# Optimization experiments

Hardware: AMD Instinct MI355X
Metric: run time of the kernel (lower is better)

Reference implementation:

```python
import jax, jax.numpy as jnp
import numpy as np


def _bilinear_align_corners(g, H, W):
    # g: [B, 1, h, w] -> [B, 1, H, W], matching F.interpolate(mode='bilinear', align_corners=True)
    B, C, h, w = g.shape
    ys = jnp.linspace(0.0, h - 1.0, H)
    xs = jnp.linspace(0.0, w - 1.0, W)
    y0 = jnp.clip(jnp.floor(ys).astype(jnp.int32), 0, h - 1)
    y1 = jnp.clip(y0 + 1, 0, h - 1)
    x0 = jnp.clip(jnp.floor(xs).astype(jnp.int32), 0, w - 1)
    x1 = jnp.clip(x0 + 1, 0, w - 1)
    wy = (ys - y0.astype(g.dtype))[:, None]          # [H,1]
    wx = (xs - x0.astype(g.dtype))[None, :]          # [1,W]
    g00 = g[:, :, y0][:, :, :, x0]                   # [B,C,H,W]
    g01 = g[:, :, y0][:, :, :, x1]
    g10 = g[:, :, y1][:, :, :, x0]
    g11 = g[:, :, y1][:, :, :, x1]
    top = g00 * (1 - wx) + g01 * wx
    bot = g10 * (1 - wx) + g11 * wx
    return top * (1 - wy) + bot * wy


def setup_inputs() -> dict:
    key = jax.random.key(0)
    ks = jax.random.split(key, 6)
    B, C, H, W = 4, 256, 64, 64
    Cq = C // 8
    return {
        "x": jax.random.normal(ks[0], (B, C, H, W), jnp.float32),
        "guiding_map0": jax.random.normal(ks[1], (B, 1, 32, 32), jnp.float32),
        "Wq": jax.random.normal(ks[2], (Cq, C), jnp.float32) * 0.05,
        "bq": jnp.zeros((Cq,), jnp.float32),
        "Wk": jax.random.normal(ks[3], (Cq, C), jnp.float32) * 0.05,
        "bk": jnp.zeros((Cq,), jnp.float32),
        "Wv": jax.random.normal(ks[4], (C, C), jnp.float32) * 0.05,
        "bv": jnp.zeros((C,), jnp.float32),
        "gamma": jnp.ones((1,), jnp.float32),
    }


def reference(x, guiding_map0, Wq, bq, Wk, bk, Wv, bv, gamma):
    B, C, H, W = x.shape
    N = H * W
    gm = jax.nn.sigmoid(_bilinear_align_corners(guiding_map0, H, W))  # [B,1,H,W]
    gate = 1.0 + gm
    # 1x1 convs as channel contractions, then multiplicative gating
    q = (jnp.einsum('oc,bchw->bohw', Wq, x) + bq[None, :, None, None]) * gate
    k = (jnp.einsum('oc,bchw->bohw', Wk, x) + bk[None, :, None, None]) * gate
    v = (jnp.einsum('oc,bchw->bohw', Wv, x) + bv[None, :, None, None]) * gate
    q = q.reshape(B, -1, N)   # [B,Cq,N]
    k = k.reshape(B, -1, N)   # [B,Cq,N]
    v = v.reshape(B, C, N)    # [B,C,N]
    energy = jnp.einsum('bcm,bcn->bmn', q, k)        # [B,N,N]
    attention = jax.nn.softmax(energy, axis=-1)
    # out[b,c,m] = sum_n v[b,c,n] * attn[b,m,n]
    out = jnp.einsum('bcn,bmn->bcm', v, attention).reshape(B, C, H, W)
    return gamma[0] * out + x
```

## Files before the change

### kernel.cpp

```cpp
#include <hip/hip_runtime.h>
#include <math.h>

#define NN 4096
#define CC 256

typedef unsigned short u16;
typedef float f32x16 __attribute__((ext_vector_type(16)));
typedef short s16x8 __attribute__((ext_vector_type(8)));

#define ZERO16 {0.f,0.f,0.f,0.f,0.f,0.f,0.f,0.f,0.f,0.f,0.f,0.f,0.f,0.f,0.f,0.f}

#define GLOAD_LDS16(gsrc, ldst) \
    __builtin_amdgcn_global_load_lds((const __attribute__((address_space(1))) unsigned int*)(gsrc), \
                                     (__attribute__((address_space(3))) unsigned int*)(ldst), 16, 0, 0)

__device__ __forceinline__ u16 f2bf(float f){
    unsigned u = __float_as_uint(f);
    return (u16)((u + 0x7fffu + ((u >> 16) & 1u)) >> 16);
}
__device__ __forceinline__ float bf2f(u16 h){
    return __uint_as_float(((unsigned)h) << 16);
}

__global__ __launch_bounds__(256) void gate_kernel(
    const float* __restrict__ g0, const float* __restrict__ Wq,
    const float* __restrict__ Wk, const float* __restrict__ Wv,
    float* __restrict__ gate,
    u16* __restrict__ wqhi, u16* __restrict__ wqlo,
    u16* __restrict__ wkhi, u16* __restrict__ wklo,
    u16* __restrict__ wvbf)
{
    int idx = blockIdx.x * 256 + threadIdx.x;
    int b  = idx >> 12;
    int hw = idx & 4095;
    int h = hw >> 6, w = hw & 63;
    float ys = h * (31.0f / 63.0f);
    float xs = w * (31.0f / 63.0f);
    int y0 = (int)ys, x0 = (int)xs;
    int y1 = min(y0 + 1, 31), x1 = min(x0 + 1, 31);
    float wy = ys - (float)y0, wx = xs - (float)x0;
    const float* g = g0 + b * 1024;
    float g00 = g[y0 * 32 + x0], g01 = g[y0 * 32 + x1];
    float g10 = g[y1 * 32 + x0], g11 = g[y1 * 32 + x1];
    float top = g00 * (1.0f - wx) + g01 * wx;
    float bot = g10 * (1.0f - wx) + g11 * wx;
    float val = top * (1.0f - wy) + bot * wy;
    gate[idx] = 1.0f + 1.0f / (1.0f + __expf(-val));

    if (idx < 8192) {
        float a = Wq[idx];
        u16 ha = f2bf(a);
        wqhi[idx] = ha; wqlo[idx] = f2bf(a - bf2f(ha));
        float c = Wk[idx];
        u16 hc = f2bf(c);
        wkhi[idx] = hc; wklo[idx] = f2bf(c - bf2f(hc));
    }
#pragma unroll
    for (int j = 0; j < 4; j++)
        wvbf[idx + j * 16384] = f2bf(Wv[idx + j * 16384]);
}

__global__ __launch_bounds__(512, 4) void qkv_kernel(
    const float* __restrict__ x,
    const u16* __restrict__ wqhi, const u16* __restrict__ wqlo,
    const u16* __restrict__ wkhi, const u16* __restrict__ wklo,
    const u16* __restrict__ wvbf,
    const float* __restrict__ bq, const float* __restrict__ bk,
    const float* __restrict__ bv, const float* __restrict__ gate,
    u16* __restrict__ qpk, u16* __restrict__ kpk,
    u16* __restrict__ vbf)
{
    __shared__ u16 Xh[64 * 256];
    __shared__ u16 Xl[64 * 256];
    int bid = blockIdx.x;
    int b  = (bid >> 1) & 3;
    int nt = (bid >> 3) | ((bid & 1) << 5);
    int n0 = nt * 64;
    int tid = threadIdx.x;

    {
        const float* xb = x + (size_t)b * CC * NN;
        int cb = tid >> 4;
        int nc = tid & 15;
#pragma unroll
        for (int j = 0; j < 8; j++) {
            int c = cb + 32 * j;
            float4 xv = *(const float4*)(xb + (size_t)c * NN + n0 + nc * 4);
            float xf[4] = {xv.x, xv.y, xv.z, xv.w};
#pragma unroll
            for (int i = 0; i < 4; i++) {
                int n = nc * 4 + i;
                u16 hv = f2bf(xf[i]);
                u16 lv = f2bf(xf[i] - bf2f(hv));
                int u = n * 256 + (c ^ ((n & 31) << 3));
                Xh[u] = hv; Xl[u] = lv;
            }
        }
    }
    __syncthreads();

    int w = tid >> 6, l = tid & 63;
    int l5 = l >> 5, l31 = l & 31;

    if (w < 4) {
        int proj = w & 1, nh = w >> 1;
        const u16* Whi = proj ? wkhi : wqhi;
        const u16* Wlo = proj ? wklo : wqlo;
        const float* bias = proj ? bk : bq;
        u16* dpk = proj ? kpk : qpk;
        int nl = nh * 32 + l31;
        int swz = (nl & 31) << 3;

        f32x16 acc = ZERO16;
        for (int ks = 0; ks < 16; ks++) {
            int c0 = ks * 16 + 8 * l5;
            s16x8 whi = *(const s16x8*)(Whi + l31 * 256 + c0);
            s16x8 wlo = *(const s16x8*)(Wlo + l31 * 256 + c0);
            int u = nl * 256 + (c0 ^ swz);
            s16x8 xh = *(const s16x8*)(Xh + u);
            s16x8 xl = *(const s16x8*)(Xl + u);
            acc = __builtin_amdgcn_mfma_f32_32x32x16_bf16(whi, xh, acc, 0, 0, 0);
            acc = __builtin_amdgcn_mfma_f32_32x32x16_bf16(whi, xl, acc, 0, 0, 0);
            acc = __builtin_amdgcn_mfma_f32_32x32x16_bf16(wlo, xh, acc, 0, 0, 0);
        }
        int n = n0 + nl;
        float g = gate[b * NN + n];
        size_t rowo = ((size_t)b * NN + n) * 64;
#pragma unroll
        for (int t = 0; t < 4; t++) {
            int ob = 8 * t + 4 * l5;
            unsigned h01 = 0, h23 = 0, l01 = 0, l23 = 0;
#pragma unroll
            for (int j = 0; j < 4; j++) {
                float v = (acc[4 * t + j] + bias[ob + j]) * g;
                u16 h = f2bf(v);
                u16 lo = f2bf(v - bf2f(h));
                if (j < 2) { h01 |= ((unsigned)h) << (16 * j); l01 |= ((unsigned)lo) << (16 * j); }
                else       { h23 |= ((unsigned)h) << (16 * (j - 2)); l23 |= ((unsigned)lo) << (16 * (j - 2)); }
            }
            *(unsigned*)(dpk + rowo + ob)          = h01;
            *(unsigned*)(dpk + rowo + ob + 2)      = h23;
            *(unsigned*)(dpk + rowo + 32 + ob)     = l01;
            *(unsigned*)(dpk + rowo + 32 + ob + 2) = l23;
        }
    } else {
        int vw = w - 4;
        int cB = vw * 64;
        int swz = (l31 & 31) << 3;
        f32x16 acc[2][2] = {{ZERO16, ZERO16}, {ZERO16, ZERO16}};
        for (int ks = 0; ks < 16; ks++) {
            int c0 = ks * 16 + 8 * l5;
            int u0 = l31 * 256 + (c0 ^ swz);
            s16x8 xh0 = *(const s16x8*)(Xh + u0);
            s16x8 xh1 = *(const s16x8*)(Xh + u0 + 32 * 256);
#pragma unroll
            for (int ct = 0; ct < 2; ct++) {
                s16x8 wv = *(const s16x8*)(wvbf + (size_t)(cB + ct * 32 + l31) * 256 + c0);
                acc[ct][0] = __builtin_amdgcn_mfma_f32_32x32x16_bf16(wv, xh0, acc[ct][0], 0, 0, 0);
                acc[ct][1] = __builtin_amdgcn_mfma_f32_32x32x16_bf16(wv, xh1, acc[ct][1], 0, 0, 0);
            }
        }
#pragma unroll
        for (int nh2 = 0; nh2 < 2; nh2++) {
            int n = n0 + nh2 * 32 + l31;
            float g = gate[b * NN + n];
#pragma unroll
            for (int ct = 0; ct < 2; ct++) {
#pragma unroll
                for (int r = 0; r < 16; r++) {
                    int c = cB + ct * 32 + (r & 3) + 8 * (r >> 2) + 4 * l5;
                    vbf[((size_t)b * CC + c) * NN + n] = f2bf((acc[ct][nh2][r] + bv[c]) * g);
                }
            }
        }
    }
}

__global__ __launch_bounds__(512, 4) void stats_kernel(
    const u16* __restrict__ qpk, const u16* __restrict__ kpk,
    float* __restrict__ lse)
{
    __shared__ float Sm[8][2][16], Ss[8][2][16];
    int bid = blockIdx.x;
    int b  = (bid >> 1) & 3;
    int mt = (bid >> 3) | ((bid & 1) << 5);
    int tid = threadIdx.x;
    int w = tid >> 6, l = tid & 63;
    int l5 = l >> 5, l31 = l & 31;
    int strip = w & 1, ns = w >> 1;
    int mS = mt * 64 + strip * 32;

    size_t qo = ((size_t)b * NN + mS + l31) * 64 + 8 * l5;
    s16x8 qh0 = *(const s16x8*)(qpk + qo),      ql0 = *(const s16x8*)(qpk + qo + 32);
    s16x8 qh1 = *(const s16x8*)(qpk + qo + 16), ql1 = *(const s16x8*)(qpk + qo + 48);

    float rmax[16], rsum[16];
#pragma unroll
    for (int r = 0; r < 16; r++) { rmax[r] = -1e30f; rsum[r] = 0.f; }

    for (int it = 0; it < 32; it++) {
        size_t ko = ((size_t)b * NN + it * 128 + ns * 32 + l31) * 64 + 8 * l5;
        s16x8 kh0 = *(const s16x8*)(kpk + ko),      kl0 = *(const s16x8*)(kpk + ko + 32);
        s16x8 kh1 = *(const s16x8*)(kpk + ko + 16), kl1 = *(const s16x8*)(kpk + ko + 48);
        f32x16 a = ZERO16;
        a = __builtin_amdgcn_mfma_f32_32x32x16_bf16(ql0, kh0, a, 0, 0, 0);
        a = __builtin_amdgcn_mfma_f32_32x32x16_bf16(qh0, kl0, a, 0, 0, 0);
        a = __builtin_amdgcn_mfma_f32_32x32x16_bf16(qh0, kh0, a, 0, 0, 0);
        a = __builtin_amdgcn_mfma_f32_32x32x16_bf16(ql1, kh1, a, 0, 0, 0);
        a = __builtin_amdgcn_mfma_f32_32x32x16_bf16(qh1, kl1, a, 0, 0, 0);
        a = __builtin_amdgcn_mfma_f32_32x32x16_bf16(qh1, kh1, a, 0, 0, 0);
#pragma unroll
        for (int r = 0; r < 16; r++) {
            float nm = fmaxf(rmax[r], a[r]);
            rsum[r] = rsum[r] * __expf(rmax[r] - nm) + __expf(a[r] - nm);
            rmax[r] = nm;
        }
    }

#pragma unroll
    for (int r = 0; r < 16; r++) {
#pragma unroll
        for (int off = 16; off >= 1; off >>= 1) {
            float om = __shfl_xor(rmax[r], off);
            float os = __shfl_xor(rsum[r], off);
            float nm = fmaxf(rmax[r], om);
            rsum[r] = rsum[r] * __expf(rmax[r] - nm) + os * __expf(om - nm);
            rmax[r] = nm;
        }
    }
    if (l31 == 0) {
#pragma unroll
        for (int r = 0; r < 16; r++) { Sm[w][l5][r] = rmax[r]; Ss[w][l5][r] = rsum[r]; }
    }
    __syncthreads();
    if (w < 2 && l31 == 0) {
#pragma unroll
        for (int r = 0; r < 16; r++) {
            float M = -1e30f;
#pragma unroll
            for (int j = 0; j < 4; j++) M = fmaxf(M, Sm[w + 2 * j][l5][r]);
            float S = 0.f;
#pragma unroll
            for (int j = 0; j < 4; j++)
                S += Ss[w + 2 * j][l5][r] * __expf(Sm[w + 2 * j][l5][r] - M);
            int m = mt * 64 + w * 32 + (r & 3) + 8 * (r >> 2) + 4 * l5;
            lse[b * NN + m] = M + __logf(S);
        }
    }
}

__global__ __launch_bounds__(512, 2) void out_kernel(
    const u16* __restrict__ qpk, const u16* __restrict__ kpk,
    const u16* __restrict__ vbf, const float* __restrict__ lse,
    const float* __restrict__ x, const float* __restrict__ gamma,
    float* __restrict__ out)
{
    __shared__ u16 Vl[128 * 128];
    __shared__ u16 Pl[64 * 128];
    int bid = blockIdx.x;
    int sub = bid & 7;
    int b  = sub >> 1;
    int ch = sub & 1;
    int mt = bid >> 3;
    int tid = threadIdx.x;
    int w = tid >> 6, l = tid & 63;
    int l5 = l >> 5, l31 = l & 31;
    int strip = w & 1, cq = w >> 1;
    int mS = mt * 64 + strip * 32;

    size_t qo = ((size_t)b * NN + mS + l31) * 64 + 8 * l5;
    s16x8 qh0 = *(const s16x8*)(qpk + qo),      ql0 = *(const s16x8*)(qpk + qo + 32);
    s16x8 qh1 = *(const s16x8*)(qpk + qo + 16), ql1 = *(const s16x8*)(qpk + qo + 48);

    float lr[16];
#pragma unroll
    for (int r = 0; r < 16; r++)
        lr[r] = lse[b * NN + mS + (r & 3) + 8 * (r >> 2) + 4 * l5];

    f32x16 acc = ZERO16;
    const u16* vb = vbf + ((size_t)b * CC + ch * 128) * NN;

    for (int it = 0; it < 32; it++) {
        int n0 = it * 128;
#pragma unroll
        for (int j = 0; j < 4; j++) {
            int s = j * 512 + w * 64 + l;
            int c = s >> 4, chk = s & 15;
            const u16* src = vb + (size_t)c * NN + n0 + ((chk * 8) ^ ((c & 15) << 3));
            GLOAD_LDS16(src, Vl + (size_t)(j * 512 + w * 64) * 8);
        }
        {
            size_t ko = ((size_t)b * NN + n0 + cq * 32 + l31) * 64 + 8 * l5;
            s16x8 kh0 = *(const s16x8*)(kpk + ko),      kl0 = *(const s16x8*)(kpk + ko + 32);
            s16x8 kh1 = *(const s16x8*)(kpk + ko + 16), kl1 = *(const s16x8*)(kpk + ko + 48);
            f32x16 a = ZERO16;
            a = __builtin_amdgcn_mfma_f32_32x32x16_bf16(ql0, kh0, a, 0, 0, 0);
            a = __builtin_amdgcn_mfma_f32_32x32x16_bf16(qh0, kl0, a, 0, 0, 0);
            a = __builtin_amdgcn_mfma_f32_32x32x16_bf16(qh0, kh0, a, 0, 0, 0);
            a = __builtin_amdgcn_mfma_f32_32x32x16_bf16(ql1, kh1, a, 0, 0, 0);
            a = __builtin_amdgcn_mfma_f32_32x32x16_bf16(qh1, kl1, a, 0, 0, 0);
            a = __builtin_amdgcn_mfma_f32_32x32x16_bf16(qh1, kh1, a, 0, 0, 0);
#pragma unroll
            for (int r = 0; r < 16; r++) {
                float p = __expf(a[r] - lr[r]);
                int m = strip * 32 + (r & 3) + 8 * (r >> 2) + 4 * l5;
                int nc = cq * 32 + l31;
                Pl[m * 128 + (nc ^ ((m & 15) << 3))] = f2bf(p);
            }
        }
        __syncthreads();
#pragma unroll
        for (int ks = 0; ks < 8; ks++) {
            int col = ks * 16 + 8 * l5;
            int mr = strip * 32 + l31;
            int cr = cq * 32 + l31;
            s16x8 pa = *(const s16x8*)(Pl + mr * 128 + (col ^ ((mr & 15) << 3)));
            s16x8 vv = *(const s16x8*)(Vl + cr * 128 + (col ^ ((cr & 15) << 3)));
            acc = __builtin_amdgcn_mfma_f32_32x32x16_bf16(pa, vv, acc, 0, 0, 0);
        }
        __syncthreads();
    }

    float gm = gamma[0];
    int c = ch * 128 + cq * 32 + l31;
#pragma unroll
    for (int t = 0; t < 4; t++) {
        size_t o = ((size_t)b * CC + c) * NN + mS + 8 * t + 4 * l5;
        float4 x4 = *(const float4*)(x + o);
        float4 r4;
        r4.x = fmaf(gm, acc[4 * t + 0], x4.x);
        r4.y = fmaf(gm, acc[4 * t + 1], x4.y);
        r4.z = fmaf(gm, acc[4 * t + 2], x4.z);
        r4.w = fmaf(gm, acc[4 * t + 3], x4.w);
        *(float4*)(out + o) = r4;
    }
}

extern "C" void kernel_launch(void* const* d_in, const int* in_sizes, int n_in,
                              void* d_out, int out_size, void* d_ws, size_t ws_size,
                              hipStream_t stream)
{
    const float* x     = (const float*)d_in[0];
    const float* g0    = (const float*)d_in[1];
    const float* Wq    = (const float*)d_in[2];
    const float* bq    = (const float*)d_in[3];
    const float* Wk    = (const float*)d_in[4];
    const float* bk    = (const float*)d_in[5];
    const float* Wv    = (const float*)d_in[6];
    const float* bv    = (const float*)d_in[7];
    const float* gamma = (const float*)d_in[8];
    float* out = (float*)d_out;

    char* p = (char*)d_ws;
    u16* qpk = (u16*)p; p += (size_t)4 * NN * 64 * 2;
    u16* kpk = (u16*)p; p += (size_t)4 * NN * 64 * 2;
    u16* vbf = (u16*)p; p += (size_t)4 * CC * NN * 2;
    float* gate = (float*)p; p += (size_t)4 * NN * 4;
    float* lse  = (float*)p; p += (size_t)4 * NN * 4;
    u16* wqhi = (u16*)p; p += 8192 * 2;
    u16* wqlo = (u16*)p; p += 8192 * 2;
    u16* wkhi = (u16*)p; p += 8192 * 2;
    u16* wklo = (u16*)p; p += 8192 * 2;
    u16* wvbf = (u16*)p; p += 65536 * 2;

    hipLaunchKernelGGL(gate_kernel, dim3(64), dim3(256), 0, stream,
                       g0, Wq, Wk, Wv, gate, wqhi, wqlo, wkhi, wklo, wvbf);
    hipLaunchKernelGGL(qkv_kernel, dim3(256), dim3(512), 0, stream,
                       x, wqhi, wqlo, wkhi, wklo, wvbf, bq, bk, bv, gate,
                       qpk, kpk, vbf);
    hipLaunchKernelGGL(stats_kernel, dim3(256), dim3(512), 0, stream,
                       qpk, kpk, lse);
    hipLaunchKernelGGL(out_kernel, dim3(512), dim3(512), 0, stream,
                       qpk, kpk, vbf, lse, x, gamma, out);
}
```

Measured before the change: 161.6 us.

## Transpose energy MFMA, fold log2e into Q, double-buffer P, read V directly

Q is pre-scaled by log2(e) so softmax can use exp2f. The energy MFMA operands are swapped so each lane holds one query row, which lets the stats kernel keep a scalar running max and sum instead of sixteen of each, and removes most shuffle reductions. In the output kernel, P is double-buffered in LDS so the next tile's energy is computed while the current PV runs, leaving one barrier per iteration. V is now loaded straight from global memory into registers rather than staged through LDS, trading LDS traffic and a barrier for uncoalesced global reads.

After: 234.9 us. +45.4%, slower.

```diff
diff --git a/kernel.cpp b/kernel.cpp
--- a/kernel.cpp
+++ b/kernel.cpp
@@ -5,14 +5,12 @@
 #define CC 256
 
 typedef unsigned short u16;
+typedef unsigned int u32;
 typedef float f32x16 __attribute__((ext_vector_type(16)));
 typedef short s16x8 __attribute__((ext_vector_type(8)));
 
 #define ZERO16 {0.f,0.f,0.f,0.f,0.f,0.f,0.f,0.f,0.f,0.f,0.f,0.f,0.f,0.f,0.f,0.f}
-
-#define GLOAD_LDS16(gsrc, ldst) \
-    __builtin_amdgcn_global_load_lds((const __attribute__((address_space(1))) unsigned int*)(gsrc), \
-                                     (__attribute__((address_space(3))) unsigned int*)(ldst), 16, 0, 0)
+#define LOG2E 1.4426950408889634f
 
 __device__ __forceinline__ u16 f2bf(float f){
     unsigned u = __float_as_uint(f);
@@ -108,6 +106,7 @@
         const u16* Wlo = proj ? wklo : wqlo;
         const float* bias = proj ? bk : bq;
         u16* dpk = proj ? kpk : qpk;
+        float scale = proj ? 1.0f : LOG2E;
         int nl = nh * 32 + l31;
         int swz = (nl & 31) << 3;
 
@@ -124,7 +123,7 @@
             acc = __builtin_amdgcn_mfma_f32_32x32x16_bf16(wlo, xh, acc, 0, 0, 0);
         }
         int n = n0 + nl;
-        float g = gate[b * NN + n];
+        float g = gate[b * NN + n] * scale;
         size_t rowo = ((size_t)b * NN + n) * 64;
 #pragma unroll
         for (int t = 0; t < 4; t++) {
@@ -180,7 +179,7 @@
     const u16* __restrict__ qpk, const u16* __restrict__ kpk,
     float* __restrict__ lse)
 {
-    __shared__ float Sm[8][2][16], Ss[8][2][16];
+    __shared__ float Sm[8][32], Ss[8][32];
     int bid = blockIdx.x;
     int b  = (bid >> 1) & 3;
     int mt = (bid >> 3) | ((bid & 1) << 5);
@@ -194,58 +193,52 @@
     s16x8 qh0 = *(const s16x8*)(qpk + qo),      ql0 = *(const s16x8*)(qpk + qo + 32);
     s16x8 qh1 = *(const s16x8*)(qpk + qo + 16), ql1 = *(const s16x8*)(qpk + qo + 48);
 
-    float rmax[16], rsum[16];
-#pragma unroll
-    for (int r = 0; r < 16; r++) { rmax[r] = -1e30f; rsum[r] = 0.f; }
+    float rmax = -1e30f, rsum = 0.f;
 
     for (int it = 0; it < 32; it++) {
         size_t ko = ((size_t)b * NN + it * 128 + ns * 32 + l31) * 64 + 8 * l5;
         s16x8 kh0 = *(const s16x8*)(kpk + ko),      kl0 = *(const s16x8*)(kpk + ko + 32);
         s16x8 kh1 = *(const s16x8*)(kpk + ko + 16), kl1 = *(const s16x8*)(kpk + ko + 48);
         f32x16 a = ZERO16;
-        a = __builtin_amdgcn_mfma_f32_32x32x16_bf16(ql0, kh0, a, 0, 0, 0);
-        a = __builtin_amdgcn_mfma_f32_32x32x16_bf16(qh0, kl0, a, 0, 0, 0);
-        a = __builtin_amdgcn_mfma_f32_32x32x16_bf16(qh0, kh0, a, 0, 0, 0);
-        a = __builtin_amdgcn_mfma_f32_32x32x16_bf16(ql1, kh1, a, 0, 0, 0);
-        a = __builtin_amdgcn_mfma_f32_32x32x16_bf16(qh1, kl1, a, 0, 0, 0);
-        a = __builtin_amdgcn_mfma_f32_32x32x16_bf16(qh1, kh1, a, 0, 0, 0);
-#pragma unroll
-        for (int r = 0; r < 16; r++) {
-            float nm = fmaxf(rmax[r], a[r]);
-            rsum[r] = rsum[r] * __expf(rmax[r] - nm) + __expf(a[r] - nm);
-            rmax[r] = nm;
-        }
-    }
-
-#pragma unroll
-    for (int r = 0; r < 16; r++) {
-#pragma unroll
-        for (int off = 16; off >= 1; off >>= 1) {
-            float om = __shfl_xor(rmax[r], off);
-            float os = __shfl_xor(rsum[r], off);
-            float nm = fmaxf(rmax[r], om);
-            rsum[r] = rsum[r] * __expf(rmax[r] - nm) + os * __expf(om - nm);
-            rmax[r] = nm;
-        }
-    }
-    if (l31 == 0) {
-#pragma unroll
-        for (int r = 0; r < 16; r++) { Sm[w][l5][r] = rmax[r]; Ss[w][l5][r] = rsum[r]; }
-    }
+        a = __builtin_amdgcn_mfma_f32_32x32x16_bf16(kh0, ql0, a, 0, 0, 0);
+        a = __builtin_amdgcn_mfma_f32_32x32x16_bf16(kl0, qh0, a, 0, 0, 0);
+        a = __builtin_amdgcn_mfma_f32_32x32x16_bf16(kh0, qh0, a, 0, 0, 0);
+        a = __builtin_amdgcn_mfma_f32_32x32x16_bf16(kh1, ql1, a, 0, 0, 0);
+        a = __builtin_amdgcn_mfma_f32_32x32x16_bf16(kl1, qh1, a, 0, 0, 0);
+        a = __builtin_amdgcn_mfma_f32_32x32x16_bf16(kh1, qh1, a, 0, 0, 0);
+        float t0 = fmaxf(fmaxf(a[0], a[1]),   fmaxf(a[2], a[3]));
+        float t1 = fmaxf(fmaxf(a[4], a[5]),   fmaxf(a[6], a[7]));
+        float t2 = fmaxf(fmaxf(a[8], a[9]),   fmaxf(a[10], a[11]));
+        float t3 = fmaxf(fmaxf(a[12], a[13]), fmaxf(a[14], a[15]));
+        float tm = fmaxf(fmaxf(t0, t1), fmaxf(t2, t3));
+        float nm = fmaxf(rmax, tm);
+        float add = 0.f;
+#pragma unroll
+        for (int r = 0; r < 16; r++) add += exp2f(a[r] - nm);
+        rsum = rsum * exp2f(rmax - nm) + add;
+        rmax = nm;
+    }
+
+    {
+        float om = __shfl_xor(rmax, 32);
+        float os = __shfl_xor(rsum, 32);
+        float nm = fmaxf(rmax, om);
+        rsum = rsum * exp2f(rmax - nm) + os * exp2f(om - nm);
+        rmax = nm;
+    }
+    if (l < 32) { Sm[w][l] = rmax; Ss[w][l] = rsum; }
     __syncthreads();
-    if (w < 2 && l31 == 0) {
-#pragma unroll
-        for (int r = 0; r < 16; r++) {
-            float M = -1e30f;
-#pragma unroll
-            for (int j = 0; j < 4; j++) M = fmaxf(M, Sm[w + 2 * j][l5][r]);
-            float S = 0.f;
-#pragma unroll
-            for (int j = 0; j < 4; j++)
-                S += Ss[w + 2 * j][l5][r] * __expf(Sm[w + 2 * j][l5][r] - M);
-            int m = mt * 64 + w * 32 + (r & 3) + 8 * (r >> 2) + 4 * l5;
-            lse[b * NN + m] = M + __logf(S);
-        }
+    if (tid < 64) {
+        int ww = tid >> 5;
+        int mm = tid & 31;
+        float M = -1e30f;
+#pragma unroll
+        for (int j = 0; j < 4; j++) M = fmaxf(M, Sm[ww + 2 * j][mm]);
+        float S = 0.f;
+#pragma unroll
+        for (int j = 0; j < 4; j++)
+            S += Ss[ww + 2 * j][mm] * exp2f(Sm[ww + 2 * j][mm] - M);
+        lse[b * NN + mt * 64 + ww * 32 + mm] = M + log2f(S);
     }
 }
 
@@ -255,8 +248,7 @@
     const float* __restrict__ x, const float* __restrict__ gamma,
     float* __restrict__ out)
 {
-    __shared__ u16 Vl[128 * 128];
-    __shared__ u16 Pl[64 * 128];
+    __shared__ u16 Pl[2][64 * 128];
     int bid = blockIdx.x;
     int sub = bid & 7;
     int b  = sub >> 1;
@@ -272,54 +264,63 @@
     s16x8 qh0 = *(const s16x8*)(qpk + qo),      ql0 = *(const s16x8*)(qpk + qo + 32);
     s16x8 qh1 = *(const s16x8*)(qpk + qo + 16), ql1 = *(const s16x8*)(qpk + qo + 48);
 
-    float lr[16];
-#pragma unroll
-    for (int r = 0; r < 16; r++)
-        lr[r] = lse[b * NN + mS + (r & 3) + 8 * (r >> 2) + 4 * l5];
+    float lse_m = lse[b * NN + mS + l31];
 
     f32x16 acc = ZERO16;
-    const u16* vb = vbf + ((size_t)b * CC + ch * 128) * NN;
-
-    for (int it = 0; it < 32; it++) {
+    const u16* vrow = vbf + ((size_t)b * CC + ch * 128 + cq * 32 + l31) * NN + 8 * l5;
+
+    int mloc = strip * 32 + l31;
+    int wbase = mloc * 256;
+    int wswz  = (mloc & 15) << 4;
+
+    auto ENERGY = [&](int it) {
         int n0 = it * 128;
-#pragma unroll
-        for (int j = 0; j < 4; j++) {
-            int s = j * 512 + w * 64 + l;
-            int c = s >> 4, chk = s & 15;
-            const u16* src = vb + (size_t)c * NN + n0 + ((chk * 8) ^ ((c & 15) << 3));
-            GLOAD_LDS16(src, Vl + (size_t)(j * 512 + w * 64) * 8);
-        }
-        {
-            size_t ko = ((size_t)b * NN + n0 + cq * 32 + l31) * 64 + 8 * l5;
-            s16x8 kh0 = *(const s16x8*)(kpk + ko),      kl0 = *(const s16x8*)(kpk + ko + 32);
-            s16x8 kh1 = *(const s16x8*)(kpk + ko + 16), kl1 = *(const s16x8*)(kpk + ko + 48);
-            f32x16 a = ZERO16;
-            a = __builtin_amdgcn_mfma_f32_32x32x16_bf16(ql0, kh0, a, 0, 0, 0);
-            a = __builtin_amdgcn_mfma_f32_32x32x16_bf16(qh0, kl0, a, 0, 0, 0);
-            a = __builtin_amdgcn_mfma_f32_32x32x16_bf16(qh0, kh0, a, 0, 0, 0);
-            a = __builtin_amdgcn_mfma_f32_32x32x16_bf16(ql1, kh1, a, 0, 0, 0);
-            a = __builtin_amdgcn_mfma_f32_32x32x16_bf16(qh1, kl1, a, 0, 0, 0);
-            a = __builtin_amdgcn_mfma_f32_32x32x16_bf16(qh1, kh1, a, 0, 0, 0);
-#pragma unroll
-            for (int r = 0; r < 16; r++) {
-                float p = __expf(a[r] - lr[r]);
-                int m = strip * 32 + (r & 3) + 8 * (r >> 2) + 4 * l5;
-                int nc = cq * 32 + l31;
-                Pl[m * 128 + (nc ^ ((m & 15) << 3))] = f2bf(p);
-            }
-        }
+        size_t ko = ((size_t)b * NN + n0 + cq * 32 + l31) * 64 + 8 * l5;
+        s16x8 kh0 = *(const s16x8*)(kpk + ko),      kl0 = *(const s16x8*)(kpk + ko + 32);
+        s16x8 kh1 = *(const s16x8*)(kpk + ko + 16), kl1 = *(const s16x8*)(kpk + ko + 48);
+        f32x16 a = ZERO16;
+        a = __builtin_amdgcn_mfma_f32_32x32x16_bf16(kh0, ql0, a, 0, 0, 0);
+        a = __builtin_amdgcn_mfma_f32_32x32x16_bf16(kl0, qh0, a, 0, 0, 0);
+        a = __builtin_amdgcn_mfma_f32_32x32x16_bf16(kh0, qh0, a, 0, 0, 0);
+        a = __builtin_amdgcn_mfma_f32_32x32x16_bf16(kh1, ql1, a, 0, 0, 0);
+        a = __builtin_amdgcn_mfma_f32_32x32x16_bf16(kl1, qh1, a, 0, 0, 0);
+        a = __builtin_amdgcn_mfma_f32_32x32x16_bf16(kh1, qh1, a, 0, 0, 0);
+        char* Pb = (char*)Pl[it & 1];
+#pragma unroll
+        for (int g = 0; g < 4; g++) {
+            u16 p0 = f2bf(exp2f(a[4 * g + 0] - lse_m));
+            u16 p1 = f2bf(exp2f(a[4 * g + 1] - lse_m));
+            u16 p2 = f2bf(exp2f(a[4 * g + 2] - lse_m));
+            u16 p3 = f2bf(exp2f(a[4 * g + 3] - lse_m));
+            uint2 pk;
+            pk.x = (u32)p0 | ((u32)p1 << 16);
+            pk.y = (u32)p2 | ((u32)p3 << 16);
+            int nb = cq * 64 + 16 * g + 8 * l5;
+            *(uint2*)(Pb + ((wbase + nb) ^ wswz)) = pk;
+        }
+    };
+
+    auto PV = [&](int it) {
+        const char* Pb = (const char*)Pl[it & 1];
+        int n0 = it * 128;
+#pragma unroll
+        for (int ks = 0; ks < 8; ks++) {
+            int cb = ks * 32 + 16 * l5;
+            s16x8 pa = *(const s16x8*)(Pb + ((wbase + cb) ^ wswz));
+            s16x8 vv = *(const s16x8*)(vrow + n0 + ks * 16);
+            acc = __builtin_amdgcn_mfma_f32_32x32x16_bf16(pa, vv, acc, 0, 0, 0);
+        }
+    };
+
+    ENERGY(0);
+    __syncthreads();
+#pragma unroll 2
+    for (int it = 0; it < 31; it++) {
+        ENERGY(it + 1);
+        PV(it);
         __syncthreads();
-#pragma unroll
-        for (int ks = 0; ks < 8; ks++) {
-            int col = ks * 16 + 8 * l5;
-            int mr = strip * 32 + l31;
-            int cr = cq * 32 + l31;
-            s16x8 pa = *(const s16x8*)(Pl + mr * 128 + (col ^ ((mr & 15) << 3)));
-            s16x8 vv = *(const s16x8*)(Vl + cr * 128 + (col ^ ((cr & 15) << 3)));
-            acc = __builtin_amdgcn_mfma_f32_32x32x16_bf16(pa, vv, acc, 0, 0, 0);
-        }
-        __syncthreads();
-    }
+    }
+    PV(31);
 
     float gm = gamma[0];
     int c = ch * 128 + cq * 32 + l31;
```
